# Kernel optimization log

Hardware: AMD Instinct MI355X
Metric: run time of the kernel (lower is better)

## Reference

```python
import jax, jax.numpy as jnp
import numpy as np

N = 32000   # nodes
E = 256000  # edges
G = 64      # graphs
IN = 64     # input feature dim
TD = 32     # time embedding dim
D = 128     # hidden dim
HEADS = 4
C = D // HEADS  # per-head channels = 32
ED = 16     # edge feature dim
L = 4       # num SBlocks
FF = 4 * D  # MLP hidden


def _ln(x, g, b):
    m = x.mean(-1, keepdims=True)
    v = ((x - m) ** 2).mean(-1, keepdims=True)
    return (x - m) / jnp.sqrt(v + 1e-5) * g + b


def _time_enc(t):
    half = TD // 2
    fac = jnp.exp(jnp.arange(half, dtype=jnp.float32) * (-jnp.log(10000.0) / (half - 1 + 1e-8)))
    ang = t.astype(jnp.float32)[:, None] * fac[None, :]
    return jnp.concatenate([jnp.sin(ang), jnp.cos(ang)], axis=-1)


def setup_inputs() -> dict:
    key = jax.random.key(0)
    ks = iter(jax.random.split(key, 64))
    nrm = lambda shape: jax.random.normal(next(ks), shape, dtype=jnp.float32) * 0.02
    x = jax.random.normal(next(ks), (N, IN), dtype=jnp.float32)
    t = jax.random.randint(next(ks), (N,), 0, 128, dtype=jnp.int32)
    edge_index = jax.random.randint(next(ks), (2, E), 0, N, dtype=jnp.int32)
    edge_attr = jax.random.normal(next(ks), (E, ED), dtype=jnp.float32)
    batch = jnp.sort(jax.random.randint(next(ks), (N,), 0, G, dtype=jnp.int32))
    p = {
        'Win': nrm((IN + TD, D)), 'b_in': jnp.zeros((D,), jnp.float32),
        'Wq': nrm((L, D, D)), 'bq': jnp.zeros((L, D), jnp.float32),
        'Wk': nrm((L, D, D)), 'bk': jnp.zeros((L, D), jnp.float32),
        'Wv': nrm((L, D, D)), 'bv': jnp.zeros((L, D), jnp.float32),
        'We': nrm((L, ED, D)), 'be': jnp.zeros((L, D), jnp.float32),
        'Wskip': nrm((L, D, D)), 'bskip': jnp.zeros((L, D), jnp.float32),
        'Wbeta': nrm((L, 3 * D)),
        'ln1_g': jnp.ones((L, D), jnp.float32), 'ln1_b': jnp.zeros((L, D), jnp.float32),
        'Wff1': nrm((L, D, FF)), 'bff1': jnp.zeros((L, FF), jnp.float32),
        'Wff2': nrm((L, FF, D)), 'bff2': jnp.zeros((L, D), jnp.float32),
        'ln2_g': jnp.ones((L, D), jnp.float32), 'ln2_b': jnp.zeros((L, D), jnp.float32),
        'Wh1': nrm((2 * D, D)), 'bh1': jnp.zeros((D,), jnp.float32),
        'Wh2': nrm((D, 2)), 'bh2': jnp.zeros((2,), jnp.float32),
    }
    return {'x': x, 't': t, 'edge_index': edge_index, 'edge_attr': edge_attr, 'batch': batch, **p}


def reference(x, t, edge_index, edge_attr, batch, Win, b_in, Wq, bq, Wk, bk, Wv, bv, We, be,
              Wskip, bskip, Wbeta, ln1_g, ln1_b, Wff1, bff1, Wff2, bff2, ln2_g, ln2_b,
              Wh1, bh1, Wh2, bh2):
    # input projection with sinusoidal time encoding
    h = jnp.concatenate([x, _time_enc(t)], axis=-1)
    h = jax.nn.relu(h @ Win + b_in)
    src, dst = edge_index[0], edge_index[1]
    for i in range(L):
        # TransformerConv (multi-head, edge_attr fused into key & value, beta skip)
        q = (h @ Wq[i] + bq[i]).reshape(N, HEADS, C)
        k = (h @ Wk[i] + bk[i]).reshape(N, HEADS, C)
        v = (h @ Wv[i] + bv[i]).reshape(N, HEADS, C)
        e = (edge_attr @ We[i] + be[i]).reshape(E, HEADS, C)
        kj = k[src] + e                     # [E,H,C] gather
        vj = v[src] + e
        alpha = (q[dst] * kj).sum(-1) / jnp.sqrt(jnp.asarray(C, h.dtype))  # [E,H]
        amax = jax.ops.segment_max(alpha, dst, num_segments=N)
        ex = jnp.exp(alpha - amax[dst])
        den = jax.ops.segment_sum(ex, dst, num_segments=N)
        w = ex / den[dst]                   # segment softmax over incoming edges
        out = jax.ops.segment_sum(vj * w[..., None], dst, num_segments=N).reshape(N, D)
        xr = h @ Wskip[i] + bskip[i]
        beta = jax.nn.sigmoid(jnp.concatenate([out, xr, out - xr], -1) @ Wbeta[i])[:, None]
        xs = beta * xr + (1.0 - beta) * out
        h = _ln(h + xs, ln1_g[i], ln1_b[i])
        ff = jax.nn.relu(h @ Wff1[i] + bff1[i]) @ Wff2[i] + bff2[i]
        h = _ln(h + ff, ln2_g[i], ln2_b[i])
    # last-timestep masked readout
    tf = t.astype(h.dtype)
    tmax = jax.ops.segment_max(tf, batch, num_segments=G)
    m = tf == tmax[batch]
    mf = m.astype(h.dtype)[:, None]
    cnt = jax.ops.segment_sum(mf, batch, num_segments=G)
    gmean = jax.ops.segment_sum(h * mf, batch, num_segments=G) / jnp.maximum(cnt, 1.0)
    gmax = jax.ops.segment_max(jnp.where(m[:, None], h, -1e30), batch, num_segments=G)
    g = jnp.concatenate([gmean, gmax], axis=-1)
    return jax.nn.relu(g @ Wh1 + bh1) @ Wh2 + bh2
```

## Files before the change

kernel.cpp:

```cpp
#include <hip/hip_runtime.h>

#define N_NODES 32000
#define N_EDGES 256000
#define N_GRAPH 64
#define NLAYER  4

typedef __attribute__((ext_vector_type(8))) short short8;
typedef __attribute__((ext_vector_type(4))) float f32x4;

__device__ __forceinline__ float bf2f(unsigned short u){
  return __uint_as_float(((unsigned int)u) << 16);
}
__device__ __forceinline__ unsigned short f2bf(float f){
  unsigned int x = __float_as_uint(f);
  x = x + 0x7fffu + ((x >> 16) & 1u);
  return (unsigned short)(x >> 16);
}
__device__ __forceinline__ float ldf(const void* p, int i, int isbf){
  if(isbf) return bf2f(((const unsigned short*)p)[i]);
  return ((const float*)p)[i];
}

__global__ void TactileGAT_43207370997900_kernel() {}

__global__ void sentinel_kernel(unsigned short* out){
  int i = blockIdx.x * 64 + threadIdx.x;
  if(i < 2 * N_GRAPH) out[i] = (unsigned short)0x4000;
}

__global__ void detect_kernel(const unsigned int* ones_words, int* flag){
  if(blockIdx.x == 0 && threadIdx.x == 0)
    flag[0] = (ones_words[0] == 0x3F800000u) ? 0 : 1;
}

__global__ void zero_kernel(int* p, int n){
  int i = blockIdx.x * 256 + threadIdx.x;
  if(i < n) p[i] = 0;
}

__global__ void deg_kernel(const int* dst, int* deg){
  int e = blockIdx.x * 256 + threadIdx.x;
  if(e < N_EDGES) atomicAdd(&deg[dst[e]], 1);
}

__global__ void blocksum_kernel(const int* deg, int* psum){
  __shared__ int s[256];
  int b = blockIdx.x, tid = threadIdx.x;
  int i = b * 256 + tid;
  s[tid] = (i < N_NODES) ? deg[i] : 0;
  __syncthreads();
  for(int off = 128; off > 0; off = off / 2){
    if(tid < off) s[tid] = s[tid] + s[tid + off];
    __syncthreads();
  }
  if(tid == 0) psum[b] = s[0];
}

__global__ void scanp_kernel(int* psum){
  __shared__ int s[128];
  int tid = threadIdx.x;
  int v = (tid < 125) ? psum[tid] : 0;
  s[tid] = v;
  __syncthreads();
  for(int off = 1; off < 128; off = off * 2){
    int tv = (tid >= off) ? s[tid - off] : 0;
    __syncthreads();
    s[tid] = s[tid] + tv;
    __syncthreads();
  }
  if(tid < 125) psum[tid] = s[tid] - v;
}

__global__ void rowptr_kernel(const int* deg, const int* psum, int* rowptr,
                              int* cursor){
  __shared__ int s[256];
  int b = blockIdx.x, tid = threadIdx.x;
  int i = b * 256 + tid;
  int v = (i < N_NODES) ? deg[i] : 0;
  s[tid] = v;
  __syncthreads();
  for(int off = 1; off < 256; off = off * 2){
    int tv = (tid >= off) ? s[tid - off] : 0;
    __syncthreads();
    s[tid] = s[tid] + tv;
    __syncthreads();
  }
  int excl = s[tid] - v + psum[b];
  if(i < N_NODES){ rowptr[i] = excl; cursor[i] = excl; }
  if(i == N_NODES - 1) rowptr[N_NODES] = excl + v;
}

__global__ void scatter_kernel(const int* dst, int* cursor, int* csr){
  int e = blockIdx.x * 256 + threadIdx.x;
  if(e < N_EDGES){
    int pos = atomicAdd(&cursor[dst[e]], 1);
    csr[pos] = e;
  }
}

__global__ void pack_kernel(const void* Wq, const void* Wk, const void* Wv,
                            const void* Wsk, const void* Wff1, const void* Wff2,
                            const int* flag, unsigned short* WTq,
                            unsigned short* WT1, unsigned short* WT2){
  int idx = blockIdx.x * 256 + threadIdx.x;
  int isbf = flag[0];
  int i = idx / 196608;
  if(i >= NLAYER) return;
  int rem = idx - i * 196608;
  int seg = rem / 65536;
  int off = rem - seg * 65536;
  if(seg == 0){
    int n = off >> 7, k = off & 127;
    int sel = n >> 7, c = n & 127;
    const void* W = (sel == 0) ? Wq : (sel == 1) ? Wk : (sel == 2) ? Wv : Wsk;
    WTq[i * 65536 + off] = f2bf(ldf(W, i * 16384 + k * 128 + c, isbf));
  } else if(seg == 1){
    int n = off >> 7, k = off & 127;
    WT1[i * 65536 + off] = f2bf(ldf(Wff1, i * 65536 + k * 512 + n, isbf));
  } else {
    int n = off >> 9, k = off & 511;
    WT2[i * 65536 + off] = f2bf(ldf(Wff2, i * 65536 + k * 128 + n, isbf));
  }
}

__global__ void input_proj_kernel(const void* x, const int* t, const void* Win,
                                  const void* b_in, const int* flag,
                                  unsigned short* h){
  __shared__ float in_s[96];
  int n = blockIdx.x, d = threadIdx.x;
  int isbf = flag[0];
  if(d < 64){
    in_s[d] = ldf(x, n * 64 + d, isbf);
  } else if(d < 96){
    int j  = d - 64;
    int jj = (j < 16) ? j : (j - 16);
    float fac = expf((float)jj * (-9.210340371976184f / 15.00000001f));
    float ang = (float)t[n] * fac;
    in_s[d] = (j < 16) ? sinf(ang) : cosf(ang);
  }
  __syncthreads();
  float acc = ldf(b_in, d, isbf);
  for(int k = 0; k < 96; k++) acc += in_s[k] * ldf(Win, k * 128 + d, isbf);
  h[n * 128 + d] = f2bf(fmaxf(acc, 0.f));
}

__global__ void gemm_frag(const unsigned short* A, const unsigned short* WT,
                          const void* bias, int boff, const int* flag,
                          int K, int nbx, void* Y, int obf, int ystride,
                          int act){
  int tid = threadIdx.x;
  int bx = blockIdx.x % nbx;
  int by = blockIdx.x / nbx;
  int m0 = by * 128, c0 = bx * 128;
  int wv = tid / 64, lane = tid % 64;
  int q = lane / 16, r = lane % 16;
  const unsigned short* Ap0 = A + (m0 + wv * 32 + r) * K + q * 8;
  const unsigned short* Ap1 = Ap0 + 16 * K;
  const unsigned short* Wp = WT + (c0 + r) * K + q * 8;
  f32x4 acc[2][8];
  for(int g = 0; g < 2; g++)
    for(int tt = 0; tt < 8; tt++)
      for(int i = 0; i < 4; i++) acc[g][tt][i] = 0.f;
  for(int k0 = 0; k0 < K; k0 += 32){
    short8 a0 = *(const short8*)(Ap0 + k0);
    short8 a1 = *(const short8*)(Ap1 + k0);
    for(int tt = 0; tt < 8; tt++){
      short8 b8 = *(const short8*)(Wp + tt * 16 * K + k0);
      acc[0][tt] = __builtin_amdgcn_mfma_f32_16x16x32_bf16(a0, b8, acc[0][tt], 0, 0, 0);
      acc[1][tt] = __builtin_amdgcn_mfma_f32_16x16x32_bf16(a1, b8, acc[1][tt], 0, 0, 0);
    }
  }
  int isbf = flag[0];
  for(int tt = 0; tt < 8; tt++){
    int c = c0 + tt * 16 + r;
    float bv = ldf(bias, boff + c, isbf);
    for(int g = 0; g < 2; g++){
      for(int i = 0; i < 4; i++){
        int row = m0 + wv * 32 + g * 16 + q * 4 + i;
        float v = acc[g][tt][i] + bv;
        if(act == 1) v = fmaxf(v, 0.f);
        if(obf) ((unsigned short*)Y)[row * ystride + c] = f2bf(v);
        else    ((float*)Y)[row * ystride + c] = v;
      }
    }
  }
}

__global__ void qkvs_frag(const unsigned short* A, const unsigned short* WTq,
                          const void* b0, const void* b1, const void* b2,
                          const void* b3, int boff, const int* flag,
                          float* qs, unsigned int* kvp){
  int tid = threadIdx.x;
  int sel = blockIdx.x % 4;
  int by  = blockIdx.x / 4;
  int m0 = by * 128;
  int wv = tid / 64, lane = tid % 64;
  int q = lane / 16, r = lane % 16;
  const unsigned short* Ap0 = A + (m0 + wv * 32 + r) * 128 + q * 8;
  const unsigned short* Ap1 = Ap0 + 16 * 128;
  const unsigned short* Wp = WTq + (sel * 128 + r) * 128 + q * 8;
  f32x4 acc[2][8];
  for(int g = 0; g < 2; g++)
    for(int tt = 0; tt < 8; tt++)
      for(int i = 0; i < 4; i++) acc[g][tt][i] = 0.f;
  for(int k0 = 0; k0 < 128; k0 += 32){
    short8 a0 = *(const short8*)(Ap0 + k0);
    short8 a1 = *(const short8*)(Ap1 + k0);
    for(int tt = 0; tt < 8; tt++){
      short8 b8 = *(const short8*)(Wp + tt * 16 * 128 + k0);
      acc[0][tt] = __builtin_amdgcn_mfma_f32_16x16x32_bf16(a0, b8, acc[0][tt], 0, 0, 0);
      acc[1][tt] = __builtin_amdgcn_mfma_f32_16x16x32_bf16(a1, b8, acc[1][tt], 0, 0, 0);
    }
  }
  int isbf = flag[0];
  const void* B = (sel == 0) ? b0 : (sel == 1) ? b1 : (sel == 2) ? b2 : b3;
  if(sel == 0 || sel == 3){
    for(int tt = 0; tt < 8; tt++){
      int cc = tt * 16 + r;
      float bv = ldf(B, boff + cc, isbf);
      for(int g = 0; g < 2; g++){
        for(int i = 0; i < 4; i++){
          int row = m0 + wv * 32 + g * 16 + q * 4 + i;
          float v = acc[g][tt][i] + bv;
          if(sel == 0) qs[row * 256 + cc] = v;
          else         qs[row * 256 + 128 + cc] = v;
        }
      }
    }
  } else {
    int base = (sel - 1) * 64;
    for(int tt = 0; tt < 4; tt++){
      int cc0 = tt * 16 + r;
      float bv0 = ldf(B, boff + cc0, isbf);
      float bv1 = ldf(B, boff + cc0 + 64, isbf);
      for(int g = 0; g < 2; g++){
        for(int i = 0; i < 4; i++){
          int row = m0 + wv * 32 + g * 16 + q * 4 + i;
          unsigned int w = (unsigned int)f2bf(acc[g][tt][i] + bv0)
                         | ((unsigned int)f2bf(acc[g][tt + 4][i] + bv1) << 16);
          kvp[row * 128 + base + cc0] = w;
        }
      }
    }
  }
}

#define CH 4
__global__ void attn_epi1_kernel(const float* qs, const unsigned int* kvp,
                                 const void* edge_attr, const int* esrc,
                                 const int* rowptr, const int* csr,
                                 const void* We, int weoff, const void* be, int beoff,
                                 const void* Wbeta, int wboff,
                                 const void* lng, int lgoff,
                                 const void* lnb, int lboff,
                                 const unsigned short* h, const int* flag,
                                 unsigned short* h2){
  __shared__ float sea[CH * 16];
  __shared__ float sprod[CH * 144];
  __shared__ float svj[CH * 128];
  __shared__ float salpha[CH * 4];
  __shared__ float red[64];
  int n = blockIdx.x, L = threadIdx.x;
  int isbf = flag[0];
  int hL = L >> 5, c = L & 31;
  float q0 = qs[n * 256 + L]      * 0.17677669529663687f;
  float q1 = qs[n * 256 + 64 + L] * 0.17677669529663687f;
  float wec0[16], wec1[16];
  for(int j = 0; j < 16; j++){
    wec0[j] = ldf(We, weoff + j * 128 + L, isbf);
    wec1[j] = ldf(We, weoff + j * 128 + 64 + L, isbf);
  }
  float be0 = ldf(be, beoff + L, isbf);
  float be1 = ldf(be, beoff + 64 + L, isbf);
  float m0 = -1e30f, l0 = 0.f, acc0 = 0.f;
  float m1 = -1e30f, l1 = 0.f, acc1 = 0.f;
  int beg = rowptr[n], end = rowptr[n + 1];
  for(int ci = beg; ci < end; ci += CH){
    int Ep = end - ci; if(Ep > CH) Ep = CH;
    for(int tt = L; tt < Ep * 16; tt += 64){
      int i = tt >> 4, j = tt & 15;
      sea[tt] = ldf(edge_attr, csr[ci + i] * 16 + j, isbf);
    }
    unsigned int kws[CH], vws[CH];
    for(int i = 0; i < CH; i++){
      if(i < Ep){
        int src = esrc[csr[ci + i]];
        kws[i] = kvp[src * 128 + L];
        vws[i] = kvp[src * 128 + 64 + L];
      }
    }
    __syncthreads();
    for(int i = 0; i < Ep; i++){
      const f32x4* sp = (const f32x4*)(sea + i * 16);
      f32x4 e0 = sp[0], e1 = sp[1], e2 = sp[2], e3 = sp[3];
      float ea[16];
      *(f32x4*)(ea + 0)  = e0; *(f32x4*)(ea + 4)  = e1;
      *(f32x4*)(ea + 8)  = e2; *(f32x4*)(ea + 12) = e3;
      float ed0 = be0, ed1 = be1;
      for(int j = 0; j < 16; j++){
        ed0 += ea[j] * wec0[j];
        ed1 += ea[j] * wec1[j];
      }
      float kd0 = bf2f((unsigned short)(kws[i] & 0xffffu)) + ed0;
      float kd1 = bf2f((unsigned short)(kws[i] >> 16)) + ed1;
      float vd0 = bf2f((unsigned short)(vws[i] & 0xffffu)) + ed0;
      float vd1 = bf2f((unsigned short)(vws[i] >> 16)) + ed1;
      sprod[i * 144 + hL * 36 + c]       = q0 * kd0;
      sprod[i * 144 + (2 + hL) * 36 + c] = q1 * kd1;
      svj[i * 128 + L]      = vd0;
      svj[i * 128 + 64 + L] = vd1;
    }
    __syncthreads();
    if(L < 16){
      int i = L >> 2, h4 = L & 3;
      if(i < Ep){
        const f32x4* pp = (const f32x4*)(sprod + i * 144 + h4 * 36);
        float s = 0.f;
        for(int tq = 0; tq < 8; tq++){
          f32x4 v4 = pp[tq];
          s += v4[0] + v4[1] + v4[2] + v4[3];
        }
        salpha[i * 4 + h4] = s;
      }
    }
    __syncthreads();
    float mc0 = -1e30f, mc1 = -1e30f;
    for(int i = 0; i < Ep; i++){
      float a0 = salpha[i * 4 + hL];
      float a1 = salpha[i * 4 + 2 + hL];
      mc0 = fmaxf(mc0, a0);
      mc1 = fmaxf(mc1, a1);
    }
    float mn0 = fmaxf(m0, mc0);
    float mn1 = fmaxf(m1, mc1);
    float sc0 = expf(m0 - mn0);
    float sc1 = expf(m1 - mn1);
    l0 = l0 * sc0; acc0 = acc0 * sc0;
    l1 = l1 * sc1; acc1 = acc1 * sc1;
    for(int i = 0; i < Ep; i++){
      float p0 = expf(salpha[i * 4 + hL] - mn0);
      float p1 = expf(salpha[i * 4 + 2 + hL] - mn1);
      l0 += p0; acc0 += p0 * svj[i * 128 + L];
      l1 += p1; acc1 += p1 * svj[i * 128 + 64 + L];
    }
    m0 = mn0; m1 = mn1;
    __syncthreads();
  }
  float o0 = (l0 > 0.f) ? acc0 / l0 : 0.f;
  float o1 = (l1 > 0.f) ? acc1 / l1 : 0.f;
  float xr0 = qs[n * 256 + 128 + L];
  float xr1 = qs[n * 256 + 192 + L];
  float hv0 = bf2f(h[n * 128 + L]);
  float hv1 = bf2f(h[n * 128 + 64 + L]);
  float part = o0 * ldf(Wbeta, wboff + L, isbf)
             + xr0 * ldf(Wbeta, wboff + 128 + L, isbf)
             + (o0 - xr0) * ldf(Wbeta, wboff + 256 + L, isbf)
             + o1 * ldf(Wbeta, wboff + 64 + L, isbf)
             + xr1 * ldf(Wbeta, wboff + 192 + L, isbf)
             + (o1 - xr1) * ldf(Wbeta, wboff + 320 + L, isbf);
  red[L] = part;
  __syncthreads();
  for(int off = 32; off > 0; off = off / 2){
    if(L < off) red[L] = red[L] + red[L + off];
    __syncthreads();
  }
  float beta = 1.f / (1.f + expf(-red[0]));
  __syncthreads();
  float y0 = hv0 + beta * xr0 + (1.f - beta) * o0;
  float y1 = hv1 + beta * xr1 + (1.f - beta) * o1;
  red[L] = y0 + y1;
  __syncthreads();
  for(int off = 32; off > 0; off = off / 2){
    if(L < off) red[L] = red[L] + red[L + off];
    __syncthreads();
  }
  float mean = red[0] * (1.f / 128.f);
  __syncthreads();
  float dy0 = y0 - mean, dy1 = y1 - mean;
  red[L] = dy0 * dy0 + dy1 * dy1;
  __syncthreads();
  for(int off = 32; off > 0; off = off / 2){
    if(L < off) red[L] = red[L] + red[L + off];
    __syncthreads();
  }
  float var = red[0] * (1.f / 128.f);
  float inv = 1.f / sqrtf(var + 1e-5f);
  h2[n * 128 + L]      = f2bf(dy0 * inv * ldf(lng, lgoff + L, isbf)
                              + ldf(lnb, lboff + L, isbf));
  h2[n * 128 + 64 + L] = f2bf(dy1 * inv * ldf(lng, lgoff + 64 + L, isbf)
                              + ldf(lnb, lboff + 64 + L, isbf));
}

__global__ void ff2_ln_kernel(const unsigned short* A, const unsigned short* WT,
                              const void* bias, int boff,
                              const unsigned short* h2,
                              const void* lng, int lgoff,
                              const void* lnb, int lboff,
                              const int* flag, unsigned short* outh){
  __shared__ float Ys[64 * 133];
  __shared__ float smean[64];
  __shared__ float sinv[64];
  int tid = threadIdx.x;
  int m0 = blockIdx.x * 64;
  int wv = tid / 64, lane = tid % 64;
  int q = lane / 16, r = lane % 16;
  const unsigned short* Ap = A + (m0 + wv * 16 + r) * 512 + q * 8;
  const unsigned short* Wp = WT + r * 512 + q * 8;
  f32x4 acc[8];
  for(int tt = 0; tt < 8; tt++)
    for(int i = 0; i < 4; i++) acc[tt][i] = 0.f;
  for(int k0 = 0; k0 < 512; k0 += 32){
    short8 a8 = *(const short8*)(Ap + k0);
    for(int tt = 0; tt < 8; tt++){
      short8 b8 = *(const short8*)(Wp + tt * 16 * 512 + k0);
      acc[tt] = __builtin_amdgcn_mfma_f32_16x16x32_bf16(a8, b8, acc[tt], 0, 0, 0);
    }
  }
  int isbf = flag[0];
  for(int tt = 0; tt < 8; tt++){
    int c = tt * 16 + r;
    float bv = ldf(bias, boff + c, isbf);
    for(int i = 0; i < 4; i++){
      int rl = wv * 16 + q * 4 + i;
      float v = acc[tt][i] + bv;
      Ys[rl * 133 + c] = bf2f(h2[(m0 + rl) * 128 + c]) + v;
    }
  }
  __syncthreads();
  if(tid < 64){
    float s = 0.f, s2 = 0.f;
    for(int c = 0; c < 128; c++){
      float y = Ys[tid * 133 + c];
      s += y; s2 += y * y;
    }
    float mean = s * (1.f / 128.f);
    float var  = s2 * (1.f / 128.f) - mean * mean;
    smean[tid] = mean;
    sinv[tid]  = 1.f / sqrtf(var + 1e-5f);
  }
  __syncthreads();
  for(int tt = 0; tt < 8; tt++){
    int c = tt * 16 + r;
    float g = ldf(lng, lgoff + c, isbf);
    float b = ldf(lnb, lboff + c, isbf);
    for(int i = 0; i < 4; i++){
      int rl = wv * 16 + q * 4 + i;
      float y = Ys[rl * 133 + c];
      outh[(m0 + rl) * 128 + c] = f2bf((y - smean[rl]) * sinv[rl] * g + b);
    }
  }
}

__global__ void bounds_kernel(const int* batch, int* gstart, int* gend){
  int n = blockIdx.x * 256 + threadIdx.x;
  if(n >= N_NODES) return;
  int b = batch[n];
  if(n == 0 || batch[n - 1] != b) gstart[b] = n;
  if(n == N_NODES - 1 || batch[n + 1] != b) gend[b] = n + 1;
}

__global__ void readout_kernel(const int* t, const unsigned short* h,
                               const int* gstart, const int* gend, float* gbuf){
  __shared__ int redi[128];
  int g = blockIdx.x, d = threadIdx.x;
  int s = gstart[g], e = gend[g];
  int tm = -2147483647;
  for(int nn = s + d; nn < e; nn += 128){
    int tv = t[nn];
    tm = (tv > tm) ? tv : tm;
  }
  redi[d] = tm;
  __syncthreads();
  for(int off = 64; off > 0; off = off / 2){
    if(d < off) redi[d] = (redi[d + off] > redi[d]) ? redi[d + off] : redi[d];
    __syncthreads();
  }
  tm = redi[0];
  float sum = 0.f, mx = -1e30f;
  int cnt = 0;
  for(int nn = s; nn < e; nn++){
    if(t[nn] == tm){
      float hv = bf2f(h[nn * 128 + d]);
      sum += hv;
      mx = fmaxf(mx, hv);
      cnt = cnt + 1;
    }
  }
  gbuf[g * 256 + d]       = sum / (float)((cnt < 1) ? 1 : cnt);
  gbuf[g * 256 + 128 + d] = mx;
}

__global__ void mlp_kernel(const float* gbuf, const void* Wh1, const void* bh1,
                           const void* Wh2, const void* bh2, const int* flag,
                           void* outp){
  __shared__ float gs[256];
  __shared__ float r1[128];
  int g = blockIdx.x, d = threadIdx.x;
  int isbf = flag[0];
  gs[d]       = gbuf[g * 256 + d];
  gs[d + 128] = gbuf[g * 256 + 128 + d];
  __syncthreads();
  float acc = ldf(bh1, d, isbf);
  for(int k = 0; k < 256; k++) acc += gs[k] * ldf(Wh1, k * 128 + d, isbf);
  r1[d] = fmaxf(acc, 0.f);
  __syncthreads();
  if(d < 2){
    float a = ldf(bh2, d, isbf);
    for(int k = 0; k < 128; k++) a += r1[k] * ldf(Wh2, k * 2 + d, isbf);
    if(isbf) ((unsigned short*)outp)[g * 2 + d] = f2bf(a);
    else     ((float*)outp)[g * 2 + d] = a;
  }
}

extern "C" void kernel_launch(void* const* d_in, const int* in_sizes, int n_in,
                              void* d_out, int out_size, void* d_ws, size_t ws_size,
                              hipStream_t stream){
  const void* x          = d_in[0];
  const int*  t          = (const int*)d_in[1];
  const int*  edge_index = (const int*)d_in[2];
  const void* edge_attr  = d_in[3];
  const int*  batch      = (const int*)d_in[4];
  const void* Win  = d_in[5];  const void* b_in = d_in[6];
  const void* Wq   = d_in[7];  const void* bq   = d_in[8];
  const void* Wk   = d_in[9];  const void* bk   = d_in[10];
  const void* Wv   = d_in[11]; const void* bv   = d_in[12];
  const void* We   = d_in[13]; const void* be   = d_in[14];
  const void* Wsk  = d_in[15]; const void* bsk  = d_in[16];
  const void* Wbeta= d_in[17];
  const void* ln1g = d_in[18]; const void* ln1b = d_in[19];
  const void* Wff1 = d_in[20]; const void* bff1 = d_in[21];
  const void* Wff2 = d_in[22]; const void* bff2 = d_in[23];
  const void* ln2g = d_in[24]; const void* ln2b = d_in[25];
  const void* Wh1  = d_in[26]; const void* bh1  = d_in[27];
  const void* Wh2  = d_in[28]; const void* bh2  = d_in[29];
  (void)in_sizes; (void)n_in; (void)out_size; (void)ws_size;

  char* p = (char*)d_ws;
  unsigned short* h    = (unsigned short*)p; p += (long long)N_NODES * 128 * 2;
  unsigned short* h2   = (unsigned short*)p; p += (long long)N_NODES * 128 * 2;
  float* qs            = (float*)p;          p += (long long)N_NODES * 256 * 4;
  unsigned int* kvp    = (unsigned int*)p;   p += (long long)N_NODES * 128 * 4;
  unsigned short* ffmid= (unsigned short*)p; p += (long long)N_NODES * 512 * 2;
  unsigned short* WTq  = (unsigned short*)p; p += (long long)NLAYER * 65536 * 2;
  unsigned short* WT1  = (unsigned short*)p; p += (long long)NLAYER * 65536 * 2;
  unsigned short* WT2  = (unsigned short*)p; p += (long long)NLAYER * 65536 * 2;
  float* gbuf = (float*)p; p += (long long)N_GRAPH * 256 * 4;
  int* flag   = (int*)p;   p += 4;
  int* rowptr = (int*)p;   p += (long long)(N_NODES + 1) * 4;
  int* cursor = (int*)p;   p += (long long)N_NODES * 4;
  int* deg    = (int*)p;   p += (long long)N_NODES * 4;
  int* gstart = (int*)p;   p += (long long)N_GRAPH * 4;
  int* gend   = (int*)p;   p += (long long)N_GRAPH * 4;
  int* psum   = (int*)p;   p += 128 * 4;
  int* csr    = (int*)p;   p += (long long)N_EDGES * 4;

  const int* esrc = edge_index;
  const int* edst = edge_index + N_EDGES;

  sentinel_kernel<<<2, 64, 0, stream>>>((unsigned short*)d_out);
  detect_kernel<<<1, 64, 0, stream>>>((const unsigned int*)ln1g, flag);

  int n_zero = N_NODES + 2 * N_GRAPH;
  zero_kernel<<<(n_zero + 255) / 256, 256, 0, stream>>>(deg, n_zero);

  pack_kernel<<<(NLAYER * 196608 + 255) / 256, 256, 0, stream>>>(
      Wq, Wk, Wv, Wsk, Wff1, Wff2, flag, WTq, WT1, WT2);
  deg_kernel<<<N_EDGES / 256, 256, 0, stream>>>(edst, deg);
  blocksum_kernel<<<125, 256, 0, stream>>>(deg, psum);
  scanp_kernel<<<1, 128, 0, stream>>>(psum);
  rowptr_kernel<<<125, 256, 0, stream>>>(deg, psum, rowptr, cursor);
  scatter_kernel<<<N_EDGES / 256, 256, 0, stream>>>(edst, cursor, csr);
  input_proj_kernel<<<N_NODES, 128, 0, stream>>>(x, t, Win, b_in, flag, h);

  int nby = N_NODES / 128;
  for(int i = 0; i < NLAYER; i++){
    qkvs_frag<<<4 * nby, 256, 0, stream>>>(
        h, WTq + (long long)i * 65536, bq, bk, bv, bsk, i * 128, flag, qs, kvp);
    attn_epi1_kernel<<<N_NODES, 64, 0, stream>>>(
        qs, kvp, edge_attr, esrc, rowptr, csr, We, i * 2048, be, i * 128,
        Wbeta, i * 384, ln1g, i * 128, ln1b, i * 128, h, flag, h2);
    gemm_frag<<<4 * nby, 256, 0, stream>>>(
        h2, WT1 + (long long)i * 65536, bff1, i * 512, flag, 128, 4,
        ffmid, 1, 512, 1);
    ff2_ln_kernel<<<N_NODES / 64, 256, 0, stream>>>(
        ffmid, WT2 + (long long)i * 65536, bff2, i * 128, h2,
        ln2g, i * 128, ln2b, i * 128, flag, h);
  }

  bounds_kernel<<<N_NODES / 256, 256, 0, stream>>>(batch, gstart, gend);
  readout_kernel<<<N_GRAPH, 128, 0, stream>>>(t, h, gstart, gend, gbuf);
  mlp_kernel<<<N_GRAPH, 128, 0, stream>>>(gbuf, Wh1, bh1, Wh2, bh2, flag, d_out);
}
```

Before: 1.045 ms.

## Use wave shuffles instead of shared memory in attention kernel, four nodes per block

The attention-plus-epilogue kernel now assigns one 64-lane wavefront per node and packs four nodes into each 256-thread block. All shared-memory staging and block barriers are removed. Per-head dot products and the LayerNorm and beta reductions now use xor shuffles, and the online softmax updates once per edge instead of in chunks of four. The aim is to cut barrier and LDS traffic and launch fewer, fuller blocks. In exchange, each lane reads the 16 edge-attribute values directly, with no cooperative load, and edge loads are serialized per edge.

```diff
diff --git a/kernel.cpp b/kernel.cpp
--- a/kernel.cpp
+++ b/kernel.cpp
@@ -245,7 +245,6 @@
   }
 }
 
-#define CH 4
 __global__ void attn_epi1_kernel(const float* qs, const unsigned int* kvp,
                                  const void* edge_attr, const int* esrc,
                                  const int* rowptr, const int* csr,
@@ -255,14 +254,10 @@
                                  const void* lnb, int lboff,
                                  const unsigned short* h, const int* flag,
                                  unsigned short* h2){
-  __shared__ float sea[CH * 16];
-  __shared__ float sprod[CH * 144];
-  __shared__ float svj[CH * 128];
-  __shared__ float salpha[CH * 4];
-  __shared__ float red[64];
-  int n = blockIdx.x, L = threadIdx.x;
-  int isbf = flag[0];
-  int hL = L >> 5, c = L & 31;
+  int wv = threadIdx.x >> 6;
+  int L  = threadIdx.x & 63;
+  int n  = blockIdx.x * 4 + wv;
+  int isbf = flag[0];
   float q0 = qs[n * 256 + L]      * 0.17677669529663687f;
   float q1 = qs[n * 256 + 64 + L] * 0.17677669529663687f;
   float wec0[16], wec1[16];
@@ -275,76 +270,38 @@
   float m0 = -1e30f, l0 = 0.f, acc0 = 0.f;
   float m1 = -1e30f, l1 = 0.f, acc1 = 0.f;
   int beg = rowptr[n], end = rowptr[n + 1];
-  for(int ci = beg; ci < end; ci += CH){
-    int Ep = end - ci; if(Ep > CH) Ep = CH;
-    for(int tt = L; tt < Ep * 16; tt += 64){
-      int i = tt >> 4, j = tt & 15;
-      sea[tt] = ldf(edge_attr, csr[ci + i] * 16 + j, isbf);
-    }
-    unsigned int kws[CH], vws[CH];
-    for(int i = 0; i < CH; i++){
-      if(i < Ep){
-        int src = esrc[csr[ci + i]];
-        kws[i] = kvp[src * 128 + L];
-        vws[i] = kvp[src * 128 + 64 + L];
-      }
-    }
-    __syncthreads();
-    for(int i = 0; i < Ep; i++){
-      const f32x4* sp = (const f32x4*)(sea + i * 16);
-      f32x4 e0 = sp[0], e1 = sp[1], e2 = sp[2], e3 = sp[3];
-      float ea[16];
-      *(f32x4*)(ea + 0)  = e0; *(f32x4*)(ea + 4)  = e1;
-      *(f32x4*)(ea + 8)  = e2; *(f32x4*)(ea + 12) = e3;
-      float ed0 = be0, ed1 = be1;
-      for(int j = 0; j < 16; j++){
-        ed0 += ea[j] * wec0[j];
-        ed1 += ea[j] * wec1[j];
-      }
-      float kd0 = bf2f((unsigned short)(kws[i] & 0xffffu)) + ed0;
-      float kd1 = bf2f((unsigned short)(kws[i] >> 16)) + ed1;
-      float vd0 = bf2f((unsigned short)(vws[i] & 0xffffu)) + ed0;
-      float vd1 = bf2f((unsigned short)(vws[i] >> 16)) + ed1;
-      sprod[i * 144 + hL * 36 + c]       = q0 * kd0;
-      sprod[i * 144 + (2 + hL) * 36 + c] = q1 * kd1;
-      svj[i * 128 + L]      = vd0;
-      svj[i * 128 + 64 + L] = vd1;
-    }
-    __syncthreads();
-    if(L < 16){
-      int i = L >> 2, h4 = L & 3;
-      if(i < Ep){
-        const f32x4* pp = (const f32x4*)(sprod + i * 144 + h4 * 36);
-        float s = 0.f;
-        for(int tq = 0; tq < 8; tq++){
-          f32x4 v4 = pp[tq];
-          s += v4[0] + v4[1] + v4[2] + v4[3];
-        }
-        salpha[i * 4 + h4] = s;
-      }
-    }
-    __syncthreads();
-    float mc0 = -1e30f, mc1 = -1e30f;
-    for(int i = 0; i < Ep; i++){
-      float a0 = salpha[i * 4 + hL];
-      float a1 = salpha[i * 4 + 2 + hL];
-      mc0 = fmaxf(mc0, a0);
-      mc1 = fmaxf(mc1, a1);
-    }
-    float mn0 = fmaxf(m0, mc0);
-    float mn1 = fmaxf(m1, mc1);
+  for(int e = beg; e < end; e++){
+    int eid = csr[e];
+    int src = esrc[eid];
+    unsigned int kw = kvp[src * 128 + L];
+    unsigned int vw = kvp[src * 128 + 64 + L];
+    float ed0 = be0, ed1 = be1;
+    for(int j = 0; j < 16; j++){
+      float s = ldf(edge_attr, eid * 16 + j, isbf);
+      ed0 += s * wec0[j];
+      ed1 += s * wec1[j];
+    }
+    float kd0 = bf2f((unsigned short)(kw & 0xffffu)) + ed0;
+    float kd1 = bf2f((unsigned short)(kw >> 16)) + ed1;
+    float vd0 = bf2f((unsigned short)(vw & 0xffffu)) + ed0;
+    float vd1 = bf2f((unsigned short)(vw >> 16)) + ed1;
+    float al0 = q0 * kd0;
+    float al1 = q1 * kd1;
+    al0 += __shfl_xor(al0, 1);  al0 += __shfl_xor(al0, 2);
+    al0 += __shfl_xor(al0, 4);  al0 += __shfl_xor(al0, 8);
+    al0 += __shfl_xor(al0, 16);
+    al1 += __shfl_xor(al1, 1);  al1 += __shfl_xor(al1, 2);
+    al1 += __shfl_xor(al1, 4);  al1 += __shfl_xor(al1, 8);
+    al1 += __shfl_xor(al1, 16);
+    float mn0 = fmaxf(m0, al0);
+    float mn1 = fmaxf(m1, al1);
     float sc0 = expf(m0 - mn0);
     float sc1 = expf(m1 - mn1);
-    l0 = l0 * sc0; acc0 = acc0 * sc0;
-    l1 = l1 * sc1; acc1 = acc1 * sc1;
-    for(int i = 0; i < Ep; i++){
-      float p0 = expf(salpha[i * 4 + hL] - mn0);
-      float p1 = expf(salpha[i * 4 + 2 + hL] - mn1);
-      l0 += p0; acc0 += p0 * svj[i * 128 + L];
-      l1 += p1; acc1 += p1 * svj[i * 128 + 64 + L];
-    }
+    float p0 = expf(al0 - mn0);
+    float p1 = expf(al1 - mn1);
+    l0 = l0 * sc0 + p0; acc0 = acc0 * sc0 + p0 * vd0;
+    l1 = l1 * sc1 + p1; acc1 = acc1 * sc1 + p1 * vd1;
     m0 = mn0; m1 = mn1;
-    __syncthreads();
   }
   float o0 = (l0 > 0.f) ? acc0 / l0 : 0.f;
   float o1 = (l1 > 0.f) ? acc1 / l1 : 0.f;
@@ -358,32 +315,23 @@
              + o1 * ldf(Wbeta, wboff + 64 + L, isbf)
              + xr1 * ldf(Wbeta, wboff + 192 + L, isbf)
              + (o1 - xr1) * ldf(Wbeta, wboff + 320 + L, isbf);
-  red[L] = part;
-  __syncthreads();
-  for(int off = 32; off > 0; off = off / 2){
-    if(L < off) red[L] = red[L] + red[L + off];
-    __syncthreads();
-  }
-  float beta = 1.f / (1.f + expf(-red[0]));
-  __syncthreads();
+  part += __shfl_xor(part, 1);  part += __shfl_xor(part, 2);
+  part += __shfl_xor(part, 4);  part += __shfl_xor(part, 8);
+  part += __shfl_xor(part, 16); part += __shfl_xor(part, 32);
+  float beta = 1.f / (1.f + expf(-part));
   float y0 = hv0 + beta * xr0 + (1.f - beta) * o0;
   float y1 = hv1 + beta * xr1 + (1.f - beta) * o1;
-  red[L] = y0 + y1;
-  __syncthreads();
-  for(int off = 32; off > 0; off = off / 2){
-    if(L < off) red[L] = red[L] + red[L + off];
-    __syncthreads();
-  }
-  float mean = red[0] * (1.f / 128.f);
-  __syncthreads();
+  float s1 = y0 + y1;
+  s1 += __shfl_xor(s1, 1);  s1 += __shfl_xor(s1, 2);
+  s1 += __shfl_xor(s1, 4);  s1 += __shfl_xor(s1, 8);
+  s1 += __shfl_xor(s1, 16); s1 += __shfl_xor(s1, 32);
+  float mean = s1 * (1.f / 128.f);
   float dy0 = y0 - mean, dy1 = y1 - mean;
-  red[L] = dy0 * dy0 + dy1 * dy1;
-  __syncthreads();
-  for(int off = 32; off > 0; off = off / 2){
-    if(L < off) red[L] = red[L] + red[L + off];
-    __syncthreads();
-  }
-  float var = red[0] * (1.f / 128.f);
+  float s2 = dy0 * dy0 + dy1 * dy1;
+  s2 += __shfl_xor(s2, 1);  s2 += __shfl_xor(s2, 2);
+  s2 += __shfl_xor(s2, 4);  s2 += __shfl_xor(s2, 8);
+  s2 += __shfl_xor(s2, 16); s2 += __shfl_xor(s2, 32);
+  float var = s2 * (1.f / 128.f);
   float inv = 1.f / sqrtf(var + 1e-5f);
   h2[n * 128 + L]      = f2bf(dy0 * inv * ldf(lng, lgoff + L, isbf)
                               + ldf(lnb, lboff + L, isbf));
@@ -576,7 +524,7 @@
   for(int i = 0; i < NLAYER; i++){
     qkvs_frag<<<4 * nby, 256, 0, stream>>>(
         h, WTq + (long long)i * 65536, bq, bk, bv, bsk, i * 128, flag, qs, kvp);
-    attn_epi1_kernel<<<N_NODES, 64, 0, stream>>>(
+    attn_epi1_kernel<<<N_NODES / 4, 256, 0, stream>>>(
         qs, kvp, edge_attr, esrc, rowptr, csr, We, i * 2048, be, i * 128,
         Wbeta, i * 384, ln1g, i * 128, ln1b, i * 128, h, flag, h2);
     gemm_frag<<<4 * nby, 256, 0, stream>>>(
```

Result: slower. 1.233 ms (+17.9%).
